# Performance work log

Hardware: AMD Instinct MI355X
Metric: run time of the kernel (lower is better)

Reference implementation:

```python
import jax, jax.numpy as jnp
import numpy as np

DILATIONS = (1, 3, 6, 12)          # layer dilations, flattened from [[1,3],[6,12]]
BLOCKS = ((0, 1), (2, 3))           # block -> layer indices
H_SIZE = 32
STATE_SIZE = 128
OUT_SIZE = STATE_SIZE - H_SIZE      # 96
INPUT_SIZE = 64
OUTPUT_SIZE = 64
T, B = 512, 512


def _linear_params(k, fan_in, fan_out):
    bound = 1.0 / np.sqrt(fan_in)
    kw, kb = jax.random.split(k)
    W = jax.random.uniform(kw, (fan_out, fan_in), minval=-bound, maxval=bound, dtype=jnp.float32)
    b = jax.random.uniform(kb, (fan_out,), minval=-bound, maxval=bound, dtype=jnp.float32)
    return W, b


def setup_inputs() -> dict:
    key = jax.random.key(0)
    ks = jax.random.split(key, 8)
    x = jax.random.normal(ks[0], (T, B, INPUT_SIZE), dtype=jnp.float32)
    ins = [INPUT_SIZE, OUT_SIZE, OUT_SIZE, OUT_SIZE]  # first layer sees raw input
    out = {"x": x}
    for l in range(4):
        W, b = _linear_params(ks[1 + l], ins[l] + 2 * H_SIZE, 4 * STATE_SIZE)
        out[f"W{l}"] = W
        out[f"b{l}"] = b
    Wa, ba = _linear_params(ks[5], OUT_SIZE, OUTPUT_SIZE)
    out["Wa"] = Wa
    out["ba"] = ba
    return out


def _s2cell(W, b, inp, prev_h, second_h, prev_c, delayed_c, has_prev, has_del):
    # xh = cat(input, prev_h, delayed_h-or-prev_h) ; zeros when no prev state (handled by caller masks)
    xh = jnp.concatenate([inp, prev_h, second_h], axis=1)
    g = xh @ W.T + b                                     # [B, 4*state]
    g0, g1, g2, g3 = jnp.split(g, 4, axis=1)
    forget = jax.nn.sigmoid(g0 + 1.0)
    cand = jnp.tanh(g1)
    alpha = jax.nn.sigmoid(g2)
    out_gate = jax.nn.sigmoid(g3)
    weighted = jnp.where(has_del, alpha * prev_c + (1.0 - alpha) * delayed_c, prev_c)
    new_c = jnp.where(has_prev, forget * weighted + (1.0 - forget) * cand, cand)
    whole = out_gate * new_c
    return whole[:, :OUT_SIZE], whole[:, OUT_SIZE:], new_c


def reference(x, W0, b0, W1, b1, W2, b2, W3, b3, Wa, ba):
    Ws = [W0, W1, W2, W3]
    bs = [b0, b1, b2, b3]
    batch = x.shape[1]
    h0 = tuple(jnp.zeros((d, batch, H_SIZE), jnp.float32) for d in DILATIONS)
    c0 = tuple(jnp.zeros((d, batch, STATE_SIZE), jnp.float32) for d in DILATIONS)

    def step(carry, inp_t):
        t, h_bufs, c_bufs = carry
        h_bufs = list(h_bufs)
        c_bufs = list(c_bufs)
        has_prev = t >= 1
        prev_block = None
        out_t = None
        for iblock, layers in enumerate(BLOCKS):
            for j, l in enumerate(layers):
                cur_in = (inp_t if iblock == 0 else prev_block) if j == 0 else out_t
                d = DILATIONS[l]
                # ring buffer: slot (t-1)%d holds state at t-1, slot t%d still holds state at t-d
                prev_h = jnp.where(has_prev, h_bufs[l][(t - 1) % d], 0.0)
                prev_c = c_bufs[l][(t - 1) % d]
                has_del = t >= d
                del_h = jnp.where(has_del, h_bufs[l][t % d], prev_h)
                del_c = c_bufs[l][t % d]
                out_t, new_h, new_c = _s2cell(Ws[l], bs[l], cur_in, prev_h, del_h,
                                              prev_c, del_c, has_prev, has_del)
                h_bufs[l] = h_bufs[l].at[t % d].set(new_h)
                c_bufs[l] = c_bufs[l].at[t % d].set(new_c)
            prev_block = out_t if iblock == 0 else out_t + prev_block  # resnet shortcut
        y = prev_block @ Wa.T + ba
        return (t + 1, tuple(h_bufs), tuple(c_bufs)), y

    _, ys = jax.lax.scan(step, (jnp.int32(0), h0, c0), x)
    return ys  # [T, B, output_size]
```

## Files before the change

### kernel.cpp

```cpp
#include <hip/hip_runtime.h>

typedef unsigned int uint;
typedef unsigned short ushort;
typedef unsigned long long u64;
typedef __attribute__((ext_vector_type(8))) short bf16x8;
typedef __attribute__((ext_vector_type(4))) float f32x4;

#define T_STEPS 512
#define BATCH   512
#define NB      8
#define RD      16
#define XS      168
#define CSTR    12
#define OUTC    96
#define FSTR    32

__device__ __forceinline__ ushort f2bf(float f){
  uint u = __builtin_bit_cast(uint, f);
  u = (u + 0x7FFFu + ((u >> 16) & 1u)) >> 16;
  return (ushort)u;
}
__device__ __forceinline__ float bf2f(ushort h){
  uint u = ((uint)h) << 16; return __builtin_bit_cast(float, u);
}
__device__ __forceinline__ float sigm(float x){
  float e = __builtin_exp2f(-1.44269504f * x);
  return __builtin_amdgcn_rcpf(1.0f + e);
}
__device__ __forceinline__ float tanh_fast(float x){
  float e = __builtin_exp2f(-2.88539008f * x);
  return 2.0f * __builtin_amdgcn_rcpf(1.0f + e) - 1.0f;
}
__device__ __forceinline__ uint aload32(const uint* p){
  return __hip_atomic_load(p, __ATOMIC_RELAXED, __HIP_MEMORY_SCOPE_AGENT);
}
__device__ __forceinline__ void astore32(uint* p, uint v){
  __hip_atomic_store(p, v, __ATOMIC_RELAXED, __HIP_MEMORY_SCOPE_AGENT);
}
__device__ __forceinline__ u64 aload64(const u64* p){
  return __hip_atomic_load(p, __ATOMIC_RELAXED, __HIP_MEMORY_SCOPE_AGENT);
}
__device__ __forceinline__ void astore64(u64* p, u64 v){
  __hip_atomic_store(p, v, __ATOMIC_RELAXED, __HIP_MEMORY_SCOPE_AGENT);
}

__global__ __launch_bounds__(512, 1)
void rnn_pipeline(const float* __restrict__ x,
                  const float* __restrict__ W0, const float* __restrict__ b0,
                  const float* __restrict__ W1, const float* __restrict__ b1,
                  const float* __restrict__ W2, const float* __restrict__ b2,
                  const float* __restrict__ W3, const float* __restrict__ b3,
                  const float* __restrict__ Wa, const float* __restrict__ ba,
                  float* __restrict__ y_out,
                  uint* __restrict__ prod, uint* __restrict__ consA,
                  uint* __restrict__ consB,
                  u64* __restrict__ hop0, u64* __restrict__ hop1,
                  u64* __restrict__ hop2)
{
  const int tid  = threadIdx.x;
  const int wv   = tid >> 6;
  const int lane = tid & 63;
  const int l15  = lane & 15;
  const int hi   = lane >> 4;
  const int rep  = blockIdx.x & 63;
  const int stage= blockIdx.x >> 6;
  const int b0r  = rep * NB;

  const int dil = (stage==0)?1:(stage==1)?3:(stage==2)?6:12;
  const int KIN = (stage==0)?64:96;
  const int K   = KIN + 64;
  const float* Wl = (stage==0)?W0:(stage==1)?W1:(stage==2)?W2:W3;
  const float* bl = (stage==0)?b0:(stage==1)?b1:(stage==2)?b2:b3;

  __shared__ __align__(16) ushort xh_hi[16*XS], xh_lo[16*XS];
  __shared__ __align__(16) float  sh_c[12*128*CSTR];
  __shared__ __align__(16) ushort h_hi[12*NB*32], h_lo[12*NB*32];
  __shared__ __align__(16) ushort outp[2304];
  __shared__ __align__(16) ushort o1p[1536];
  __shared__ __align__(16) float  o3f[NB*OUTC];

  for (int i = tid; i < 16*XS; i += 512){ xh_hi[i] = 0; xh_lo[i] = 0; }
  for (int i = tid; i < 12*128*CSTR; i += 512) sh_c[i] = 0.0f;
  for (int i = tid; i < 12*NB*32; i += 512){ h_hi[i] = 0; h_lo[i] = 0; }
  for (int i = tid; i < 2304; i += 512) outp[i] = 0;
  for (int i = tid; i < 1536; i += 512) o1p[i] = 0;
  for (int i = tid; i < NB*OUTC; i += 512) o3f[i] = 0.0f;

  const int sidx = 16*wv + l15;

  bf16x8 whi[4][5], wlo[4][5];
  #pragma unroll
  for (int j = 0; j < 4; ++j){
    const int grow = 128*j + sidx;
    #pragma unroll
    for (int ks = 0; ks < 5; ++ks){
      bf16x8 vh, vl;
      const int cb = ks*32 + hi*8;
      if (cb < K){
        const float* p = Wl + (size_t)grow*K + cb;
        #pragma unroll
        for (int i = 0; i < 8; ++i){
          float w = p[i];
          ushort h = f2bf(w);
          vh[i] = (short)h;
          vl[i] = (short)f2bf(w - bf2f(h));
        }
      } else {
        #pragma unroll
        for (int i = 0; i < 8; ++i){ vh[i] = 0; vl[i] = 0; }
      }
      whi[j][ks] = vh; wlo[j][ks] = vl;
    }
  }
  float bias[4];
  #pragma unroll
  for (int j = 0; j < 4; ++j) bias[j] = bl[128*j + sidx];

  bf16x8 phi[3], plo[3];
  #pragma unroll
  for (int ks = 0; ks < 3; ++ks){
    bf16x8 z;
    #pragma unroll
    for (int i = 0; i < 8; ++i) z[i]=0;
    phi[ks]=z; plo[ks]=z;
  }
  float bav = 0.0f;
  if (stage == 3 && wv < 4){
    const int ocol = 16*wv + l15;
    #pragma unroll
    for (int ks = 0; ks < 3; ++ks){
      const float* p = Wa + (size_t)ocol*96 + ks*32 + hi*8;
      bf16x8 vh, vl;
      #pragma unroll
      for (int i = 0; i < 8; ++i){
        float w = p[i];
        ushort h = f2bf(w);
        vh[i] = (short)h;
        vl[i] = (short)f2bf(w - bf2f(h));
      }
      phi[ks] = vh; plo[ks] = vl;
    }
    bav = ba[ocol];
  }

  uint* up_prod  = (stage==1)? &prod[rep*FSTR] : (stage==2)? &prod[(64+rep)*FSTR] :
                   (stage==3)? &prod[(128+rep)*FSTR] : nullptr;
  uint* up_prod1 = (stage==3)? &prod[(64+rep)*FSTR] : nullptr;
  uint* my_prod  = (stage==0)? &prod[rep*FSTR] : (stage==1)? &prod[(64+rep)*FSTR] :
                   (stage==2)? &prod[(128+rep)*FSTR] : nullptr;
  uint* my_consA = (stage==1)? &consA[rep*FSTR] : (stage==2)? &consA[(64+rep)*FSTR] :
                   (stage==3)? &consA[(128+rep)*FSTR] : nullptr;
  uint* my_consB = (stage==3)? &consB[rep*FSTR] : nullptr;
  uint* dnA      = (stage==0)? &consA[rep*FSTR] : (stage==1)? &consA[(64+rep)*FSTR] :
                   (stage==2)? &consA[(128+rep)*FSTR] : nullptr;
  uint* dnB      = (stage==1)? &consB[rep*FSTR] : nullptr;
  const u64* hop_in  = (stage==1)? hop0 : (stage==2)? hop1 : nullptr;
  u64*       hop_out = (stage==0)? hop0 : (stage==1)? hop1 : (stage==2)? hop2 : nullptr;

  __syncthreads();

  u64 pfA = 0, pfB = 0; float xv = 0.0f;
  if (stage == 0){
    const int r = tid >> 6, c = tid & 63;
    xv = x[(size_t)(b0r + r)*64 + c];
  } else if (stage < 3){
    uint f = aload32(up_prod);
    while (f < 1u){ __builtin_amdgcn_s_sleep(2); f = aload32(up_prod); }
    if (tid < 384) pfA = aload64(hop_in + (size_t)rep*384 + tid);
  } else {
    uint f = aload32(up_prod);
    while (f < 1u){ __builtin_amdgcn_s_sleep(2); f = aload32(up_prod); }
    f = aload32(up_prod1);
    while (f < 1u){ __builtin_amdgcn_s_sleep(2); f = aload32(up_prod1); }
    const u64* s2 = hop2 + (size_t)rep*384;
    const u64* s1 = hop1 + (size_t)rep*384;
    pfA = (tid < 384) ? aload64(s2 + tid) : aload64(s1 + (tid - 384));
    if (tid < 256) pfB = aload64(s1 + 128 + tid);
  }

  int cur = 0, prv = dil - 1;
  for (int t = 0; t < T_STEPS; ++t){
    const int slot = t & (RD-1);

    asm volatile("s_waitcnt vmcnt(0)" ::: "memory");
    if (stage == 0){
      const int r = tid >> 6, c = tid & 63;
      ushort hb = f2bf(xv);
      xh_hi[r*XS + c] = hb;
      xh_lo[r*XS + c] = f2bf(xv - bf2f(hb));
    } else {
      if (tid < 384){
        const int q = (tid < 192) ? tid : tid - 192;
        ushort* plane = (tid < 192) ? xh_hi : xh_lo;
        const int r = q / 24, c4 = (q % 24) * 4;
        *(u64*)(plane + r*XS + c4) = pfA;
      } else if (stage == 3){
        *(u64*)(o1p + 4*(tid - 384)) = pfA;
      }
      if (stage == 3 && tid < 256) *(u64*)(o1p + 4*(128 + tid)) = pfB;
    }
    {
      const int which = tid >> 8, rem = tid & 255, r = rem >> 5, c = rem & 31;
      const int srcslot = (which == 1 && t >= dil) ? cur : prv;
      xh_hi[r*XS + KIN + which*32 + c] = h_hi[srcslot*(NB*32) + r*32 + c];
      xh_lo[r*XS + KIN + which*32 + c] = h_lo[srcslot*(NB*32) + r*32 + c];
    }
    __syncthreads();
    if (tid == 0){
      if (stage > 0){
        astore32(my_consA, (uint)(t+1));
        if (stage == 3) astore32(my_consB, (uint)(t+1));
      }
      if (stage < 3 && t > 0) astore32(my_prod, (uint)t);
    }
    const bool pre = (t + 1 < T_STEPS);
    uint up_f = 0, up_f1 = 0, dn_f = 0, dn_fB = 0;
    if (pre && stage > 0)  up_f  = aload32(up_prod);
    if (pre && stage == 3) up_f1 = aload32(up_prod1);
    if (stage < 3)         dn_f  = aload32(dnA);
    if (stage == 1)        dn_fB = aload32(dnB);

    f32x4 acc[4];
    #pragma unroll
    for (int j = 0; j < 4; ++j) acc[j] = (f32x4){bias[j],bias[j],bias[j],bias[j]};
    const int abase = l15*XS + hi*8;
    #pragma unroll
    for (int ks = 0; ks < 5; ++ks){
      if (ks*32 < K){
        bf16x8 ahi = *(const bf16x8*)(xh_hi + abase + ks*32);
        bf16x8 alo = *(const bf16x8*)(xh_lo + abase + ks*32);
        #pragma unroll
        for (int j = 0; j < 4; ++j){
          acc[j] = __builtin_amdgcn_mfma_f32_16x16x32_bf16(ahi, whi[j][ks], acc[j], 0, 0, 0);
          acc[j] = __builtin_amdgcn_mfma_f32_16x16x32_bf16(alo, whi[j][ks], acc[j], 0, 0, 0);
          acc[j] = __builtin_amdgcn_mfma_f32_16x16x32_bf16(ahi, wlo[j][ks], acc[j], 0, 0, 0);
        }
      }
    }

    if (pre){
      if (stage == 0){
        const int r = tid >> 6, c = tid & 63;
        xv = x[(size_t)((t+1)*BATCH + b0r + r)*64 + c];
      } else {
        const uint need = (uint)(t + 2);
        while (up_f < need){ __builtin_amdgcn_s_sleep(2); up_f = aload32(up_prod); }
        if (stage == 3)
          while (up_f1 < need){ __builtin_amdgcn_s_sleep(2); up_f1 = aload32(up_prod1); }
        const int ns = (t + 1) & (RD-1);
        if (stage < 3){
          if (tid < 384) pfA = aload64(hop_in + (size_t)(ns*64 + rep)*384 + tid);
        } else {
          const u64* s2 = hop2 + (size_t)(ns*64 + rep)*384;
          const u64* s1 = hop1 + (size_t)(ns*64 + rep)*384;
          pfA = (tid < 384) ? aload64(s2 + tid) : aload64(s1 + (tid - 384));
          if (tid < 256) pfB = aload64(s1 + 128 + tid);
        }
      }
    }

    f32x4 pc = *(const f32x4*)(sh_c + prv*(128*CSTR) + sidx*CSTR + hi*4);
    f32x4 dc = *(const f32x4*)(sh_c + cur*(128*CSTR) + sidx*CSTR + hi*4);
    const bool has_prev = (t >= 1), has_del = (t >= dil);
    f32x4 ncv; float whv[4];
    #pragma unroll
    for (int k = 0; k < 4; ++k){
      float f  = sigm(acc[0][k] + 1.0f);
      float cd = tanh_fast(acc[1][k]);
      float al = sigm(acc[2][k]);
      float og = sigm(acc[3][k]);
      float wt = has_del ? (al*pc[k] + (1.0f - al)*dc[k]) : pc[k];
      float nc = has_prev ? (f*wt + (1.0f - f)*cd) : cd;
      ncv[k] = nc;
      whv[k] = og * nc;
    }
    if (hi < 2){
      *(f32x4*)(sh_c + cur*(128*CSTR) + sidx*CSTR + hi*4) = ncv;
      #pragma unroll
      for (int k = 0; k < 4; ++k){
        const int r = hi*4 + k;
        const float w = whv[k];
        if (sidx < OUTC){
          if (stage == 3){
            o3f[r*OUTC + sidx] = w;
          } else {
            ushort hb = f2bf(w);
            outp[r*OUTC + sidx]       = hb;
            outp[768 + r*OUTC + sidx] = f2bf(w - bf2f(hb));
          }
        } else {
          ushort hb = f2bf(w);
          h_hi[cur*(NB*32) + r*32 + (sidx - OUTC)] = hb;
          h_lo[cur*(NB*32) + r*32 + (sidx - OUTC)] = f2bf(w - bf2f(hb));
        }
      }
    }
    __syncthreads();

    if (stage < 3){
      if (t >= RD){
        const uint need = (uint)(t - RD + 1);
        while (dn_f < need){ __builtin_amdgcn_s_sleep(2); dn_f = aload32(dnA); }
        if (stage == 1)
          while (dn_fB < need){ __builtin_amdgcn_s_sleep(2); dn_fB = aload32(dnB); }
      }
      if (tid < 384){
        u64 v = *(const u64*)(outp + 4*tid);
        astore64(hop_out + (size_t)(slot*64 + rep)*384 + tid, v);
      }
    } else {
      for (int j = tid; j < 768; j += 512){
        float v = o3f[j] + bf2f(o1p[j]) + bf2f(o1p[768 + j]);
        ushort hb = f2bf(v);
        outp[j]       = hb;
        outp[768 + j] = f2bf(v - bf2f(hb));
      }
      __syncthreads();
      if (wv < 4){
        f32x4 acc1 = (f32x4){bav, bav, bav, bav};
        const int pbase = l15*96 + hi*8;
        #pragma unroll
        for (int ks = 0; ks < 3; ++ks){
          bf16x8 ahi = *(const bf16x8*)(outp + pbase + ks*32);
          bf16x8 alo = *(const bf16x8*)(outp + 768 + pbase + ks*32);
          acc1 = __builtin_amdgcn_mfma_f32_16x16x32_bf16(ahi, phi[ks], acc1, 0, 0, 0);
          acc1 = __builtin_amdgcn_mfma_f32_16x16x32_bf16(alo, phi[ks], acc1, 0, 0, 0);
          acc1 = __builtin_amdgcn_mfma_f32_16x16x32_bf16(ahi, plo[ks], acc1, 0, 0, 0);
        }
        if (hi < 2){
          const int ocol = 16*wv + l15;
          #pragma unroll
          for (int k = 0; k < 4; ++k){
            const int r = hi*4 + k;
            y_out[(size_t)(t*BATCH + b0r + r)*64 + ocol] = acc1[k];
          }
        }
      }
    }
    prv = cur;
    cur = (cur + 1 == dil) ? 0 : cur + 1;
  }

  asm volatile("s_waitcnt vmcnt(0)" ::: "memory");
  __syncthreads();
  if (stage < 3 && tid == 0) astore32(my_prod, (uint)(T_STEPS + 2));
}

extern "C" void kernel_launch(void* const* d_in, const int* in_sizes, int n_in,
                              void* d_out, int out_size, void* d_ws, size_t ws_size,
                              hipStream_t stream) {
  (void)in_sizes; (void)n_in; (void)out_size; (void)ws_size;
  const float* x  = (const float*)d_in[0];
  const float* W0 = (const float*)d_in[1];
  const float* b0 = (const float*)d_in[2];
  const float* W1 = (const float*)d_in[3];
  const float* b1 = (const float*)d_in[4];
  const float* W2 = (const float*)d_in[5];
  const float* b2 = (const float*)d_in[6];
  const float* W3 = (const float*)d_in[7];
  const float* b3 = (const float*)d_in[8];
  const float* Wa = (const float*)d_in[9];
  const float* ba = (const float*)d_in[10];
  float* out = (float*)d_out;

  uint* prod  = (uint*)d_ws;
  uint* consA = (uint*)((char*)d_ws + 24576);
  uint* consB = (uint*)((char*)d_ws + 49152);
  u64* hop0 = (u64*)((char*)d_ws + 65536);
  u64* hop1 = hop0 + (size_t)RD*64*384;
  u64* hop2 = hop1 + (size_t)RD*64*384;

  hipMemsetAsync(d_ws, 0, 65536, stream);
  hipLaunchKernelGGL(rnn_pipeline, dim3(256), dim3(512), 0, stream,
                     x, W0, b0, W1, b1, W2, b2, W3, b3, Wa, ba,
                     out, prod, consA, consB, hop0, hop1, hop2);
}
```

Baseline: 2.200 ms.

## Speculatively prefetch next-step hop data and validate flags after the fact

The per-step spin-wait on upstream producer flags before prefetching the next step's inputs is replaced by an unconditional early prefetch of the next slot's hop data plus a flag read. At the top of the next step the flag is checked, and only if it is insufficient does lane 0 spin and the data get reloaded. The producer flag is published one step later (t-1) to keep a safety margin. The output y is staged through shared memory and written one step later, and hop stores are spread across all waves (48 lanes each). The aim is to remove blocking spin-waits and serialized global traffic from the recurrent critical path, at the cost of subtle memory-ordering risk. Only lane 0 waits in the slow path, and the weakened vmcnt wait could allow stale reads.

```diff
diff --git a/kernel.cpp b/kernel.cpp
--- a/kernel.cpp
+++ b/kernel.cpp
@@ -78,6 +78,7 @@
   __shared__ __align__(16) ushort outp[2304];
   __shared__ __align__(16) ushort o1p[1536];
   __shared__ __align__(16) float  o3f[NB*OUTC];
+  __shared__ __align__(16) float  yst[512];
 
   for (int i = tid; i < 16*XS; i += 512){ xh_hi[i] = 0; xh_lo[i] = 0; }
   for (int i = tid; i < 12*128*CSTR; i += 512) sh_c[i] = 0.0f;
@@ -160,18 +161,15 @@
   __syncthreads();
 
   u64 pfA = 0, pfB = 0; float xv = 0.0f;
+  uint fvU = 0, fvU1 = 0, fvDA = 0, fvDB = 0;
   if (stage == 0){
-    const int r = tid >> 6, c = tid & 63;
-    xv = x[(size_t)(b0r + r)*64 + c];
+    xv = x[(size_t)(b0r + (tid>>6))*64 + (tid&63)];
   } else if (stage < 3){
-    uint f = aload32(up_prod);
-    while (f < 1u){ __builtin_amdgcn_s_sleep(2); f = aload32(up_prod); }
+    do { fvU = aload32(up_prod); if (fvU < 3u) __builtin_amdgcn_s_sleep(2); } while (fvU < 3u);
     if (tid < 384) pfA = aload64(hop_in + (size_t)rep*384 + tid);
   } else {
-    uint f = aload32(up_prod);
-    while (f < 1u){ __builtin_amdgcn_s_sleep(2); f = aload32(up_prod); }
-    f = aload32(up_prod1);
-    while (f < 1u){ __builtin_amdgcn_s_sleep(2); f = aload32(up_prod1); }
+    do { fvU  = aload32(up_prod);  if (fvU  < 3u) __builtin_amdgcn_s_sleep(2); } while (fvU  < 3u);
+    do { fvU1 = aload32(up_prod1); if (fvU1 < 3u) __builtin_amdgcn_s_sleep(2); } while (fvU1 < 3u);
     const u64* s2 = hop2 + (size_t)rep*384;
     const u64* s1 = hop1 + (size_t)rep*384;
     pfA = (tid < 384) ? aload64(s2 + tid) : aload64(s1 + (tid - 384));
@@ -182,7 +180,25 @@
   for (int t = 0; t < T_STEPS; ++t){
     const int slot = t & (RD-1);
 
-    asm volatile("s_waitcnt vmcnt(0)" ::: "memory");
+    if (stage < 3) asm volatile("s_waitcnt vmcnt(1)" ::: "memory");
+    if (stage > 0){
+      const bool bad = (fvU < (uint)(t+3)) || (stage==3 && fvU1 < (uint)(t+3));
+      if (bad){
+        if (lane == 0){
+          while (aload32(up_prod) < (uint)(t+1)) __builtin_amdgcn_s_sleep(2);
+          if (stage == 3)
+            while (aload32(up_prod1) < (uint)(t+1)) __builtin_amdgcn_s_sleep(2);
+        }
+        if (stage < 3){
+          if (tid < 384) pfA = aload64(hop_in + (size_t)(slot*64 + rep)*384 + tid);
+        } else {
+          const u64* s2 = hop2 + (size_t)(slot*64 + rep)*384;
+          const u64* s1 = hop1 + (size_t)(slot*64 + rep)*384;
+          pfA = (tid < 384) ? aload64(s2 + tid) : aload64(s1 + (tid - 384));
+          if (tid < 256) pfB = aload64(s1 + 128 + tid);
+        }
+      }
+    }
     if (stage == 0){
       const int r = tid >> 6, c = tid & 63;
       ushort hb = f2bf(xv);
@@ -211,14 +227,31 @@
         astore32(my_consA, (uint)(t+1));
         if (stage == 3) astore32(my_consB, (uint)(t+1));
       }
-      if (stage < 3 && t > 0) astore32(my_prod, (uint)t);
+      if (stage < 3 && t >= 1) astore32(my_prod, (uint)(t-1));
+    }
+    if (stage == 3 && t > 0){
+      y_out[(size_t)((t-1)*BATCH + b0r + (tid>>6))*64 + (tid&63)] = yst[tid];
     }
     const bool pre = (t + 1 < T_STEPS);
-    uint up_f = 0, up_f1 = 0, dn_f = 0, dn_fB = 0;
-    if (pre && stage > 0)  up_f  = aload32(up_prod);
-    if (pre && stage == 3) up_f1 = aload32(up_prod1);
-    if (stage < 3)         dn_f  = aload32(dnA);
-    if (stage == 1)        dn_fB = aload32(dnB);
+    if (pre){
+      const int ns = (t + 1) & (RD-1);
+      if (stage == 0){
+        xv = x[(size_t)((t+1)*BATCH + b0r + (tid>>6))*64 + (tid&63)];
+      } else if (stage < 3){
+        if (tid < 384) pfA = aload64(hop_in + (size_t)(ns*64 + rep)*384 + tid);
+        fvU = aload32(up_prod);
+      } else {
+        const u64* s2 = hop2 + (size_t)(ns*64 + rep)*384;
+        const u64* s1 = hop1 + (size_t)(ns*64 + rep)*384;
+        pfA = (tid < 384) ? aload64(s2 + tid) : aload64(s1 + (tid - 384));
+        if (tid < 256) pfB = aload64(s1 + 128 + tid);
+        fvU  = aload32(up_prod);
+        fvU1 = aload32(up_prod1);
+      }
+    }
+    if (stage < 3) fvDA = aload32(dnA);
+    if (stage == 1) fvDB = aload32(dnB);
+    asm volatile("" ::: "memory");
 
     f32x4 acc[4];
     #pragma unroll
@@ -238,29 +271,8 @@
       }
     }
 
-    if (pre){
-      if (stage == 0){
-        const int r = tid >> 6, c = tid & 63;
-        xv = x[(size_t)((t+1)*BATCH + b0r + r)*64 + c];
-      } else {
-        const uint need = (uint)(t + 2);
-        while (up_f < need){ __builtin_amdgcn_s_sleep(2); up_f = aload32(up_prod); }
-        if (stage == 3)
-          while (up_f1 < need){ __builtin_amdgcn_s_sleep(2); up_f1 = aload32(up_prod1); }
-        const int ns = (t + 1) & (RD-1);
-        if (stage < 3){
-          if (tid < 384) pfA = aload64(hop_in + (size_t)(ns*64 + rep)*384 + tid);
-        } else {
-          const u64* s2 = hop2 + (size_t)(ns*64 + rep)*384;
-          const u64* s1 = hop1 + (size_t)(ns*64 + rep)*384;
-          pfA = (tid < 384) ? aload64(s2 + tid) : aload64(s1 + (tid - 384));
-          if (tid < 256) pfB = aload64(s1 + 128 + tid);
-        }
-      }
-    }
-
-    f32x4 pc = *(const f32x4*)(sh_c + prv*(128*CSTR) + sidx*CSTR + hi*4);
-    f32x4 dc = *(const f32x4*)(sh_c + cur*(128*CSTR) + sidx*CSTR + hi*4);
+    f32x4 pc = *(const f32x4*)(sh_c + prv*(128*CSTR) + sidx*CSTR + (hi&1)*4);
+    f32x4 dc = *(const f32x4*)(sh_c + cur*(128*CSTR) + sidx*CSTR + (hi&1)*4);
     const bool has_prev = (t >= 1), has_del = (t >= dil);
     f32x4 ncv; float whv[4];
     #pragma unroll
@@ -299,14 +311,19 @@
 
     if (stage < 3){
       if (t >= RD){
-        const uint need = (uint)(t - RD + 1);
-        while (dn_f < need){ __builtin_amdgcn_s_sleep(2); dn_f = aload32(dnA); }
-        if (stage == 1)
-          while (dn_fB < need){ __builtin_amdgcn_s_sleep(2); dn_fB = aload32(dnB); }
-      }
-      if (tid < 384){
-        u64 v = *(const u64*)(outp + 4*tid);
-        astore64(hop_out + (size_t)(slot*64 + rep)*384 + tid, v);
+        const bool badc = (fvDA < (uint)(t-13)) || (stage==1 && fvDB < (uint)(t-13));
+        if (badc){
+          if (lane == 0){
+            while (aload32(dnA) < (uint)(t-15)) __builtin_amdgcn_s_sleep(2);
+            if (stage == 1)
+              while (aload32(dnB) < (uint)(t-15)) __builtin_amdgcn_s_sleep(2);
+          }
+        }
+      }
+      if (lane < 48){
+        const int g = wv*48 + lane;
+        u64 v = *(const u64*)(outp + 4*g);
+        astore64(hop_out + (size_t)(slot*64 + rep)*384 + g, v);
       }
     } else {
       for (int j = tid; j < 768; j += 512){
@@ -331,8 +348,7 @@
           const int ocol = 16*wv + l15;
           #pragma unroll
           for (int k = 0; k < 4; ++k){
-            const int r = hi*4 + k;
-            y_out[(size_t)(t*BATCH + b0r + r)*64 + ocol] = acc1[k];
+            yst[(hi*4 + k)*64 + ocol] = acc1[k];
           }
         }
       }
@@ -343,7 +359,10 @@
 
   asm volatile("s_waitcnt vmcnt(0)" ::: "memory");
   __syncthreads();
-  if (stage < 3 && tid == 0) astore32(my_prod, (uint)(T_STEPS + 2));
+  if (stage == 3){
+    y_out[(size_t)((T_STEPS-1)*BATCH + b0r + (tid>>6))*64 + (tid&63)] = yst[tid];
+  }
+  if (stage < 3 && tid == 0) astore32(my_prod, (uint)(T_STEPS + 3));
 }
 
 extern "C" void kernel_launch(void* const* d_in, const int* in_sizes, int n_in,
```

New measurement: 2.228 ms. Within noise of the previous version (+1.2%).

## Size hop ring buffers from workspace and defer final-stage output stores

Applied to the files above, without the earlier changes.

The ring depth of the inter-stage hop buffers is now chosen at launch from the available workspace, up to 512 slots instead of a fixed 16. With a deep enough ring, producers rarely wait on downstream consumers, and the consumer-flag loads are skipped until the ring could wrap. The last stage stages its y output in shared memory and writes it to global memory one step later, so those stores overlap the next step's work. The cost is more workspace and an extra shared buffer. Correctness depends on rd staying a power of two, since the slot index is computed with a mask.

```diff
diff --git a/kernel.cpp b/kernel.cpp
--- a/kernel.cpp
+++ b/kernel.cpp
@@ -9,7 +9,6 @@
 #define T_STEPS 512
 #define BATCH   512
 #define NB      8
-#define RD      16
 #define XS      168
 #define CSTR    12
 #define OUTC    96
@@ -55,7 +54,7 @@
                   uint* __restrict__ prod, uint* __restrict__ consA,
                   uint* __restrict__ consB,
                   u64* __restrict__ hop0, u64* __restrict__ hop1,
-                  u64* __restrict__ hop2)
+                  u64* __restrict__ hop2, int rd)
 {
   const int tid  = threadIdx.x;
   const int wv   = tid >> 6;
@@ -65,6 +64,7 @@
   const int rep  = blockIdx.x & 63;
   const int stage= blockIdx.x >> 6;
   const int b0r  = rep * NB;
+  const int rmask= rd - 1;
 
   const int dil = (stage==0)?1:(stage==1)?3:(stage==2)?6:12;
   const int KIN = (stage==0)?64:96;
@@ -78,6 +78,7 @@
   __shared__ __align__(16) ushort outp[2304];
   __shared__ __align__(16) ushort o1p[1536];
   __shared__ __align__(16) float  o3f[NB*OUTC];
+  __shared__ __align__(16) float  yst[512];
 
   for (int i = tid; i < 16*XS; i += 512){ xh_hi[i] = 0; xh_lo[i] = 0; }
   for (int i = tid; i < 12*128*CSTR; i += 512) sh_c[i] = 0.0f;
@@ -85,6 +86,7 @@
   for (int i = tid; i < 2304; i += 512) outp[i] = 0;
   for (int i = tid; i < 1536; i += 512) o1p[i] = 0;
   for (int i = tid; i < NB*OUTC; i += 512) o3f[i] = 0.0f;
+  yst[tid] = 0.0f;
 
   const int sidx = 16*wv + l15;
 
@@ -160,9 +162,9 @@
   __syncthreads();
 
   u64 pfA = 0, pfB = 0; float xv = 0.0f;
+  uint fvU = 0, fvU1 = 0, fvDA = 0, fvDB = 0;
   if (stage == 0){
-    const int r = tid >> 6, c = tid & 63;
-    xv = x[(size_t)(b0r + r)*64 + c];
+    xv = x[(size_t)(b0r + (tid>>6))*64 + (tid&63)];
   } else if (stage < 3){
     uint f = aload32(up_prod);
     while (f < 1u){ __builtin_amdgcn_s_sleep(2); f = aload32(up_prod); }
@@ -180,7 +182,7 @@
 
   int cur = 0, prv = dil - 1;
   for (int t = 0; t < T_STEPS; ++t){
-    const int slot = t & (RD-1);
+    const int slot = t & rmask;
 
     asm volatile("s_waitcnt vmcnt(0)" ::: "memory");
     if (stage == 0){
@@ -211,14 +213,17 @@
         astore32(my_consA, (uint)(t+1));
         if (stage == 3) astore32(my_consB, (uint)(t+1));
       }
-      if (stage < 3 && t > 0) astore32(my_prod, (uint)t);
+      if (stage < 3 && t >= 1) astore32(my_prod, (uint)t);
+    }
+    if (stage == 3 && t > 0){
+      y_out[(size_t)((t-1)*BATCH + b0r + (tid>>6))*64 + (tid&63)] = yst[tid];
     }
     const bool pre = (t + 1 < T_STEPS);
-    uint up_f = 0, up_f1 = 0, dn_f = 0, dn_fB = 0;
+    uint up_f = 0, up_f1 = 0;
     if (pre && stage > 0)  up_f  = aload32(up_prod);
     if (pre && stage == 3) up_f1 = aload32(up_prod1);
-    if (stage < 3)         dn_f  = aload32(dnA);
-    if (stage == 1)        dn_fB = aload32(dnB);
+    if (stage < 3 && t >= rd)  fvDA = aload32(dnA);
+    if (stage == 1 && t >= rd) fvDB = aload32(dnB);
 
     f32x4 acc[4];
     #pragma unroll
@@ -240,14 +245,13 @@
 
     if (pre){
       if (stage == 0){
-        const int r = tid >> 6, c = tid & 63;
-        xv = x[(size_t)((t+1)*BATCH + b0r + r)*64 + c];
+        xv = x[(size_t)((t+1)*BATCH + b0r + (tid>>6))*64 + (tid&63)];
       } else {
         const uint need = (uint)(t + 2);
         while (up_f < need){ __builtin_amdgcn_s_sleep(2); up_f = aload32(up_prod); }
         if (stage == 3)
           while (up_f1 < need){ __builtin_amdgcn_s_sleep(2); up_f1 = aload32(up_prod1); }
-        const int ns = (t + 1) & (RD-1);
+        const int ns = (t + 1) & rmask;
         if (stage < 3){
           if (tid < 384) pfA = aload64(hop_in + (size_t)(ns*64 + rep)*384 + tid);
         } else {
@@ -259,8 +263,8 @@
       }
     }
 
-    f32x4 pc = *(const f32x4*)(sh_c + prv*(128*CSTR) + sidx*CSTR + hi*4);
-    f32x4 dc = *(const f32x4*)(sh_c + cur*(128*CSTR) + sidx*CSTR + hi*4);
+    f32x4 pc = *(const f32x4*)(sh_c + prv*(128*CSTR) + sidx*CSTR + (hi&1)*4);
+    f32x4 dc = *(const f32x4*)(sh_c + cur*(128*CSTR) + sidx*CSTR + (hi&1)*4);
     const bool has_prev = (t >= 1), has_del = (t >= dil);
     f32x4 ncv; float whv[4];
     #pragma unroll
@@ -298,11 +302,11 @@
     __syncthreads();
 
     if (stage < 3){
-      if (t >= RD){
-        const uint need = (uint)(t - RD + 1);
-        while (dn_f < need){ __builtin_amdgcn_s_sleep(2); dn_f = aload32(dnA); }
+      if (t >= rd){
+        const uint need = (uint)(t - rd + 1);
+        while (fvDA < need){ __builtin_amdgcn_s_sleep(2); fvDA = aload32(dnA); }
         if (stage == 1)
-          while (dn_fB < need){ __builtin_amdgcn_s_sleep(2); dn_fB = aload32(dnB); }
+          while (fvDB < need){ __builtin_amdgcn_s_sleep(2); fvDB = aload32(dnB); }
       }
       if (tid < 384){
         u64 v = *(const u64*)(outp + 4*tid);
@@ -331,8 +335,7 @@
           const int ocol = 16*wv + l15;
           #pragma unroll
           for (int k = 0; k < 4; ++k){
-            const int r = hi*4 + k;
-            y_out[(size_t)(t*BATCH + b0r + r)*64 + ocol] = acc1[k];
+            yst[(hi*4 + k)*64 + ocol] = acc1[k];
           }
         }
       }
@@ -343,13 +346,16 @@
 
   asm volatile("s_waitcnt vmcnt(0)" ::: "memory");
   __syncthreads();
+  if (stage == 3){
+    y_out[(size_t)((T_STEPS-1)*BATCH + b0r + (tid>>6))*64 + (tid&63)] = yst[tid];
+  }
   if (stage < 3 && tid == 0) astore32(my_prod, (uint)(T_STEPS + 2));
 }
 
 extern "C" void kernel_launch(void* const* d_in, const int* in_sizes, int n_in,
                               void* d_out, int out_size, void* d_ws, size_t ws_size,
                               hipStream_t stream) {
-  (void)in_sizes; (void)n_in; (void)out_size; (void)ws_size;
+  (void)in_sizes; (void)n_in; (void)out_size;
   const float* x  = (const float*)d_in[0];
   const float* W0 = (const float*)d_in[1];
   const float* b0 = (const float*)d_in[2];
@@ -363,15 +369,21 @@
   const float* ba = (const float*)d_in[10];
   float* out = (float*)d_out;
 
+  int rd = 16;
+  if (ws_size > 65536){
+    size_t avail = ws_size - 65536;
+    while (rd < 512 && (size_t)(rd * 2) * 64 * 9216 <= avail) rd *= 2;
+  }
+
   uint* prod  = (uint*)d_ws;
   uint* consA = (uint*)((char*)d_ws + 24576);
   uint* consB = (uint*)((char*)d_ws + 49152);
   u64* hop0 = (u64*)((char*)d_ws + 65536);
-  u64* hop1 = hop0 + (size_t)RD*64*384;
-  u64* hop2 = hop1 + (size_t)RD*64*384;
+  u64* hop1 = hop0 + (size_t)rd*64*384;
+  u64* hop2 = hop1 + (size_t)rd*64*384;
 
   hipMemsetAsync(d_ws, 0, 65536, stream);
   hipLaunchKernelGGL(rnn_pipeline, dim3(256), dim3(512), 0, stream,
                      x, W0, b0, W1, b1, W2, b2, W3, b3, Wa, ba,
-                     out, prod, consA, consB, hop0, hop1, hop2);
-}
+                     out, prod, consA, consB, hop0, hop1, hop2, rd);
+}
```

Result: no change. 2.205 ms (+0.2%).
